# Performance work log

Hardware: AMD Instinct MI355X
Metric: run time of the kernel (lower is better)

## Reference

```python
import jax, jax.numpy as jnp
import numpy as np

N, D, H, B, TOPK, M, NLAB = 200000, 512, 512, 256, 2, 100, 2000

def setup_inputs():
    rng = np.random.default_rng(0)
    features = rng.standard_normal((N, D)).astype(np.float32) * 0.05
    labels = rng.integers(0, NLAB, size=N).astype(np.int32)
    # fixed-shape cluster membership table (replaces dynamic features[labels==lab]
    # + randperm subsampling to max_cluster_num=100 in the torch loop)
    order = np.argsort(labels, kind='stable').astype(np.int32)
    counts = np.bincount(labels, minlength=NLAB)
    offs = np.concatenate([[0], np.cumsum(counts)]).astype(np.int64)
    cluster_members = np.zeros((NLAB, M), np.int32)
    cluster_mask = np.zeros((NLAB, M), np.bool_)
    for c in range(NLAB):
        k = int(min(counts[c], M))
        cluster_members[c, :k] = order[offs[c]:offs[c] + k]
        cluster_mask[c, :k] = True
    indexes = rng.integers(0, N, size=B).astype(np.int32)
    # neighbors guaranteed != indexes so neighbor labels are never the -1 placeholder
    neighbors = ((indexes[:, None] + 1 + rng.integers(0, N - 1, size=(B, TOPK))) % N).astype(np.int32)
    all_pred = rng.random((B, TOPK)).astype(np.float32)
    # GraphConv weight [2D,H] (cat(self, agg)), classifier Linear-PReLU-Linear(2)
    W1 = (rng.standard_normal((2 * D, H)) / np.sqrt(2 * D)).astype(np.float32)
    b1 = np.zeros(H, np.float32)
    W2 = (rng.standard_normal((H, H)) / np.sqrt(H)).astype(np.float32)
    b2 = np.zeros(H, np.float32)
    prelu_a = np.full(H, 0.25, np.float32)  # PReLU default init
    W3 = (rng.standard_normal((H, 2)) / np.sqrt(H)).astype(np.float32)
    b3 = np.zeros(2, np.float32)
    arrs = dict(features=features, labels=labels, indexes=indexes, neighbors=neighbors,
                all_pred=all_pred, cluster_members=cluster_members, cluster_mask=cluster_mask,
                W1=W1, b1=b1, W2=W2, b2=b2, prelu_a=prelu_a, W3=W3, b3=b3)
    return {k: jnp.asarray(v) for k, v in arrs.items()}

def _gcnl_loss(features, labels, indexes, neighbors, all_pred, cluster_members, cluster_mask,
               W1, b1, W2, b2, prelu_a, W3, b3):
    Bn = indexes.shape[0]
    sel = all_pred >= all_pred[:, :1]                    # neighbor kept if pred[:topk] >= pred[0]
    cand = labels[neighbors]                             # [B,2] candidate labels
    dup = (cand[:, 1] == cand[:, 0]) & sel[:, 0]         # torch.unique over the <=2 selected labels
    valid = jnp.stack([sel[:, 0], sel[:, 1] & ~dup], axis=1)  # [B,2]
    members = cluster_members[cand]                      # [B,2,M]
    # labels[indexes[i]] = -1 in the loop => sample never in its own cluster
    mmask = cluster_mask[cand] & (members != indexes[:, None, None])
    mfeats = features[members] * mmask[..., None].astype(features.dtype)  # [B,2,M,D] zero-padded
    x0 = features[indexes]                               # [B,D]
    x0k = jnp.broadcast_to(x0[:, None, None, :], (Bn, TOPK, 1, x0.shape[-1]))
    x = jnp.concatenate([x0k, mfeats], axis=2)           # [B,2,M+1,D] = cat(self, cluster)
    # adj = x @ x.T ; only row 0 feeds the loss (pred[0]), zero-padded rows contribute 0
    a0 = jnp.einsum('bkd,bkmd->bkm', x[:, :, 0], x)      # [B,2,M+1] adjacency row 0
    agg0 = jnp.einsum('bkm,bkmd->bkd', a0, x)            # MeanAggregator (A @ x) row 0
    cat0 = jnp.concatenate([x[:, :, 0], agg0], axis=-1)  # [B,2,2D]
    h0 = jax.nn.relu(jnp.einsum('bkd,df->bkf', cat0, W1) + b1)  # GraphConv row 0
    z = jnp.einsum('bkf,fg->bkg', h0, W2) + b2
    z = jnp.where(z >= 0, z, prelu_a * z)                # PReLU
    logits = jnp.einsum('bkg,gc->bkc', z, W3) + b3       # [B,2,2]
    gt = (cand == -1).astype(jnp.int32)                  # labels[idx] was -1 during the loop
    logp = jax.nn.log_softmax(logits, axis=-1)
    ce = -jnp.take_along_axis(logp, gt[..., None], axis=-1)[..., 0]  # [B,2]
    loss = jnp.sum(ce * valid.astype(ce.dtype)) / Bn
    return loss * 10.0

def reference(features, labels, indexes, neighbors, all_pred, cluster_members, cluster_mask,
              W1, b1, W2, b2, prelu_a, W3, b3):
    return _gcnl_loss(features, labels, indexes, neighbors, all_pred, cluster_members, cluster_mask,
                      W1, b1, W2, b2, prelu_a, W3, b3)
```

## Files before the change

### kernel.cpp

```cpp
#include <hip/hip_runtime.h>
#include <math.h>

#define N_PTS 200000
#define D 512
#define H 512
#define BATCH 256
#define TOPK 2
#define MCAP 100
#define NLAB 2000

typedef __attribute__((ext_vector_type(8))) short bf16x8;
typedef __attribute__((ext_vector_type(4))) float f32x4;

__device__ inline unsigned short f2bf(float f) {
    unsigned int u = __float_as_uint(f);
    u += 0x7FFFu + ((u >> 16) & 1u);
    return (unsigned short)(u >> 16);
}

__global__ __launch_bounds__(512) void gather_prep_kernel(
    const float* __restrict__ features, const int* __restrict__ labels,
    const int* __restrict__ indexes, const int* __restrict__ neighbors,
    const float* __restrict__ all_pred, const int* __restrict__ cluster_members,
    const float* __restrict__ W1, const float* __restrict__ W2,
    unsigned short* __restrict__ W1t, unsigned short* __restrict__ W2t,
    unsigned short* __restrict__ cat0, float* __restrict__ validf, int* __restrict__ gts,
    float* __restrict__ out)
{
    int bid = blockIdx.x;
    int tid = threadIdx.x;

    if (bid >= 512) {
        __shared__ float tt[2][32][33];
        int t = (bid - 512) * 2 + (tid >> 8);
        int t256 = tid & 255;
        int tx = t256 & 31, ty = t256 >> 5;
        const float* src; unsigned short* dst; int R, C, bi;
        if (t < 512) { src = W1; dst = W1t; R = 1024; C = 512; bi = t; }
        else         { src = W2; dst = W2t; R = 512;  C = 512; bi = t - 512; }
        int nbc = C >> 5;
        int br = (bi / nbc) * 32, bc = (bi % nbc) * 32;
        int half = tid >> 8;
        #pragma unroll
        for (int i = 0; i < 32; i += 8)
            tt[half][ty + i][tx] = src[(size_t)(br + ty + i) * C + bc + tx];
        __syncthreads();
        #pragma unroll
        for (int i = 0; i < 32; i += 8)
            dst[(size_t)(bc + ty + i) * R + br + tx] = f2bf(tt[half][tx][ty + i]);
        return;
    }

    int bk = bid;
    int b = bk >> 1, k = bk & 1;
    int lane = tid & 63, w = tid >> 6;

    if (bk == 0 && tid == 0) out[0] = 0.0f;

    int idx  = indexes[b];
    int nb   = neighbors[b * TOPK + k];
    int c    = labels[nb];
    int lab0 = labels[0];

    const float4* frow0 = (const float4*)(features + (size_t)idx * D);
    float4 x0a = frow0[lane * 2];
    float4 x0b = frow0[lane * 2 + 1];

    float agg[8] = {0,0,0,0,0,0,0,0};

    for (int m = w; m < MCAP + 1; m += 8) {
        int row;
        if (m == 0) {
            row = idx;
        } else {
            int mm = m - 1;
            int r2 = cluster_members[c * MCAP + mm];
            if (r2 == 0 && !(c == lab0 && mm == 0)) continue;
            if (r2 == idx) continue;
            row = r2;
        }
        const float4* fr = (const float4*)(features + (size_t)row * D);
        float4 fa = fr[lane * 2];
        float4 fb = fr[lane * 2 + 1];
        float p = fa.x*x0a.x + fa.y*x0a.y + fa.z*x0a.z + fa.w*x0a.w
                + fb.x*x0b.x + fb.y*x0b.y + fb.z*x0b.z + fb.w*x0b.w;
        #pragma unroll
        for (int off = 32; off >= 1; off >>= 1) p += __shfl_xor(p, off);
        agg[0] += p * fa.x; agg[1] += p * fa.y; agg[2] += p * fa.z; agg[3] += p * fa.w;
        agg[4] += p * fb.x; agg[5] += p * fb.y; agg[6] += p * fb.z; agg[7] += p * fb.w;
    }

    __shared__ float aggl[8][D];
    #pragma unroll
    for (int j = 0; j < 8; ++j) aggl[w][lane * 8 + j] = agg[j];
    __syncthreads();

    unsigned short* crow = cat0 + (size_t)bk * (2 * D);
    if (w == 0) {
        union { unsigned short u[8]; uint4 q; } pk;
        pk.u[0] = f2bf(x0a.x); pk.u[1] = f2bf(x0a.y); pk.u[2] = f2bf(x0a.z); pk.u[3] = f2bf(x0a.w);
        pk.u[4] = f2bf(x0b.x); pk.u[5] = f2bf(x0b.y); pk.u[6] = f2bf(x0b.z); pk.u[7] = f2bf(x0b.w);
        ((uint4*)crow)[lane] = pk.q;
    }
    {
        int d = tid;
        float v = aggl[0][d] + aggl[1][d] + aggl[2][d] + aggl[3][d]
                + aggl[4][d] + aggl[5][d] + aggl[6][d] + aggl[7][d];
        crow[D + d] = f2bf(v);
    }
    if (tid == 0) {
        float p0 = all_pred[b * TOPK];
        float pk = all_pred[b * TOPK + k];
        int cand0 = labels[neighbors[b * TOPK]];
        bool valid;
        if (k == 0) valid = true;
        else        valid = (pk >= p0) && (c != cand0);
        validf[bk] = valid ? 1.0f : 0.0f;
        gts[bk] = (c == -1) ? 1 : 0;
    }
}

__global__ __launch_bounds__(512) void gemm_bf16(
    const unsigned short* __restrict__ A, const unsigned short* __restrict__ Bt,
    const float* __restrict__ bias, int N, int K, int act,
    const float* __restrict__ pa, float* __restrict__ Cf, unsigned short* __restrict__ Cb)
{
    int tid = threadIdx.x;
    int lane = tid & 63, w = tid >> 6;
    int nbn = N >> 5;
    int row0 = (blockIdx.x / nbn) * 32, col0 = (blockIdx.x % nbn) * 32;

    int r = lane & 15;
    int kg = (lane >> 4) * 8;
    int kb = w * (K >> 3);

    const unsigned short* Ar0 = A  + (size_t)(row0 + r) * K + kb + kg;
    const unsigned short* Ar1 = Ar0 + (size_t)16 * K;
    const unsigned short* Br0 = Bt + (size_t)(col0 + r) * K + kb + kg;
    const unsigned short* Br1 = Br0 + (size_t)16 * K;

    f32x4 acc00 = {0,0,0,0}, acc01 = {0,0,0,0}, acc10 = {0,0,0,0}, acc11 = {0,0,0,0};

    int kchunk = K >> 3;
    for (int ks = 0; ks < kchunk; ks += 32) {
        bf16x8 a0 = *(const bf16x8*)(Ar0 + ks);
        bf16x8 a1 = *(const bf16x8*)(Ar1 + ks);
        bf16x8 b0 = *(const bf16x8*)(Br0 + ks);
        bf16x8 b1 = *(const bf16x8*)(Br1 + ks);
        acc00 = __builtin_amdgcn_mfma_f32_16x16x32_bf16(a0, b0, acc00, 0, 0, 0);
        acc01 = __builtin_amdgcn_mfma_f32_16x16x32_bf16(a0, b1, acc01, 0, 0, 0);
        acc10 = __builtin_amdgcn_mfma_f32_16x16x32_bf16(a1, b0, acc10, 0, 0, 0);
        acc11 = __builtin_amdgcn_mfma_f32_16x16x32_bf16(a1, b1, acc11, 0, 0, 0);
    }

    __shared__ float red[8][32][33];
    int rbase = (lane >> 4) * 4, cbase = lane & 15;
    #pragma unroll
    for (int j = 0; j < 4; ++j) {
        red[w][rbase + j][cbase]           = acc00[j];
        red[w][rbase + j][16 + cbase]      = acc01[j];
        red[w][16 + rbase + j][cbase]      = acc10[j];
        red[w][16 + rbase + j][16 + cbase] = acc11[j];
    }
    __syncthreads();

    for (int e = tid; e < 1024; e += 512) {
        int rr = e >> 5, cc = e & 31;
        float v = red[0][rr][cc] + red[1][rr][cc] + red[2][rr][cc] + red[3][rr][cc]
                + red[4][rr][cc] + red[5][rr][cc] + red[6][rr][cc] + red[7][rr][cc];
        int gc = col0 + cc;
        v += bias[gc];
        if (act == 0) {
            v = fmaxf(v, 0.f);
            Cb[(size_t)(row0 + rr) * N + gc] = f2bf(v);
        } else {
            v = (v >= 0.f) ? v : pa[gc] * v;
            Cf[(size_t)(row0 + rr) * N + gc] = v;
        }
    }
}

__global__ __launch_bounds__(256) void final_kernel(
    const float* __restrict__ z, const float* __restrict__ W3, const float* __restrict__ b3,
    const float* __restrict__ validf, const int* __restrict__ gts, float* __restrict__ out)
{
    int w = threadIdx.x >> 6, lane = threadIdx.x & 63;
    int bk = blockIdx.x * 4 + w;
    const float* zr = z + (size_t)bk * H;
    const float4* z4 = (const float4*)zr;
    float4 za = z4[lane * 2], zb = z4[lane * 2 + 1];
    const float4* w4 = (const float4*)W3;
    float l0 = 0, l1 = 0;
    float4 wp;
    wp = w4[lane * 4 + 0]; l0 += za.x * wp.x + za.y * wp.z; l1 += za.x * wp.y + za.y * wp.w;
    wp = w4[lane * 4 + 1]; l0 += za.z * wp.x + za.w * wp.z; l1 += za.z * wp.y + za.w * wp.w;
    wp = w4[lane * 4 + 2]; l0 += zb.x * wp.x + zb.y * wp.z; l1 += zb.x * wp.y + zb.y * wp.w;
    wp = w4[lane * 4 + 3]; l0 += zb.z * wp.x + zb.w * wp.z; l1 += zb.z * wp.y + zb.w * wp.w;
    #pragma unroll
    for (int off = 32; off >= 1; off >>= 1) {
        l0 += __shfl_xor(l0, off);
        l1 += __shfl_xor(l1, off);
    }
    if (lane == 0) {
        l0 += b3[0]; l1 += b3[1];
        int gt = gts[bk];
        float mx = fmaxf(l0, l1);
        float lse = mx + logf(expf(l0 - mx) + expf(l1 - mx));
        float sel = (gt == 0) ? l0 : l1;
        float ce = lse - sel;
        atomicAdd(out, ce * validf[bk] * (10.0f / (float)BATCH));
    }
}

extern "C" void kernel_launch(void* const* d_in, const int* in_sizes, int n_in,
                              void* d_out, int out_size, void* d_ws, size_t ws_size,
                              hipStream_t stream) {
    const float* features        = (const float*)d_in[0];
    const int*   labels          = (const int*)d_in[1];
    const int*   indexes         = (const int*)d_in[2];
    const int*   neighbors       = (const int*)d_in[3];
    const float* all_pred        = (const float*)d_in[4];
    const int*   cluster_members = (const int*)d_in[5];
    const float* W1 = (const float*)d_in[7];
    const float* b1 = (const float*)d_in[8];
    const float* W2 = (const float*)d_in[9];
    const float* b2 = (const float*)d_in[10];
    const float* pa = (const float*)d_in[11];
    const float* W3 = (const float*)d_in[12];
    const float* b3 = (const float*)d_in[13];
    float* out = (float*)d_out;

    char* ws = (char*)d_ws;
    float*          validf = (float*)(ws + 8192);
    int*            gts    = (int*)(ws + 10240);
    unsigned short* W1t    = (unsigned short*)(ws + 12288);
    unsigned short* W2t    = (unsigned short*)(ws + 1060864);
    unsigned short* cat0b  = (unsigned short*)(ws + 1585152);
    unsigned short* h0b    = (unsigned short*)(ws + 2633728);
    float*          zbuf   = (float*)(ws + 3158016);

    gather_prep_kernel<<<896, 512, 0, stream>>>(
        features, labels, indexes, neighbors, all_pred, cluster_members,
        W1, W2, W1t, W2t, cat0b, validf, gts, out);
    gemm_bf16<<<256, 512, 0, stream>>>(cat0b, W1t, b1, 512, 1024, 0, pa, nullptr, h0b);
    gemm_bf16<<<256, 512, 0, stream>>>(h0b,   W2t, b2, 512, 512,  1, pa, zbuf, nullptr);
    final_kernel<<<128, 256, 0, stream>>>(zbuf, W3, b3, validf, gts, out);
}
```

Baseline: 42.08 us.

## Fuse classifier head and loss into second GEMM with last-block reduction

Removes the final kernel and the fp32 z buffer. The second GEMM epilogue now applies PReLU, multiplies by W3, and atomically accumulates per-row logits. A last-block-done counter then computes the cross-entropy and writes the loss directly. It also specializes the GEMMs with compile-time N and K and unrolls the k loop. The cost is many global atomics on logits plus a grid-wide fence and counter, which risk contention and make the float summation order nondeterministic.

```diff
diff --git a/kernel.cpp b/kernel.cpp
--- a/kernel.cpp
+++ b/kernel.cpp
@@ -7,7 +7,6 @@
 #define BATCH 256
 #define TOPK 2
 #define MCAP 100
-#define NLAB 2000
 
 typedef __attribute__((ext_vector_type(8))) short bf16x8;
 typedef __attribute__((ext_vector_type(4))) float f32x4;
@@ -25,7 +24,7 @@
     const float* __restrict__ W1, const float* __restrict__ W2,
     unsigned short* __restrict__ W1t, unsigned short* __restrict__ W2t,
     unsigned short* __restrict__ cat0, float* __restrict__ validf, int* __restrict__ gts,
-    float* __restrict__ out)
+    float* __restrict__ logits, int* __restrict__ done)
 {
     int bid = blockIdx.x;
     int tid = threadIdx.x;
@@ -55,7 +54,11 @@
     int b = bk >> 1, k = bk & 1;
     int lane = tid & 63, w = tid >> 6;
 
-    if (bk == 0 && tid == 0) out[0] = 0.0f;
+    if (bk == 0) {
+        logits[tid] = 0.0f;
+        logits[tid + 512] = 0.0f;
+        if (tid == 0) *done = 0;
+    }
 
     int idx  = indexes[b];
     int nb   = neighbors[b * TOPK + k];
@@ -103,10 +106,9 @@
         ((uint4*)crow)[lane] = pk.q;
     }
     {
-        int d = tid;
-        float v = aggl[0][d] + aggl[1][d] + aggl[2][d] + aggl[3][d]
-                + aggl[4][d] + aggl[5][d] + aggl[6][d] + aggl[7][d];
-        crow[D + d] = f2bf(v);
+        float v = aggl[0][tid] + aggl[1][tid] + aggl[2][tid] + aggl[3][tid]
+                + aggl[4][tid] + aggl[5][tid] + aggl[6][tid] + aggl[7][tid];
+        crow[D + tid] = f2bf(v);
     }
     if (tid == 0) {
         float p0 = all_pred[b * TOPK];
@@ -120,15 +122,14 @@
     }
 }
 
-__global__ __launch_bounds__(512) void gemm_bf16(
+__global__ __launch_bounds__(512) void gemm1_kernel(
     const unsigned short* __restrict__ A, const unsigned short* __restrict__ Bt,
-    const float* __restrict__ bias, int N, int K, int act,
-    const float* __restrict__ pa, float* __restrict__ Cf, unsigned short* __restrict__ Cb)
+    const float* __restrict__ bias, unsigned short* __restrict__ Cb)
 {
+    const int N = 512, K = 1024;
     int tid = threadIdx.x;
     int lane = tid & 63, w = tid >> 6;
-    int nbn = N >> 5;
-    int row0 = (blockIdx.x / nbn) * 32, col0 = (blockIdx.x % nbn) * 32;
+    int row0 = (blockIdx.x >> 4) * 32, col0 = (blockIdx.x & 15) * 32;
 
     int r = lane & 15;
     int kg = (lane >> 4) * 8;
@@ -141,8 +142,8 @@
 
     f32x4 acc00 = {0,0,0,0}, acc01 = {0,0,0,0}, acc10 = {0,0,0,0}, acc11 = {0,0,0,0};
 
-    int kchunk = K >> 3;
-    for (int ks = 0; ks < kchunk; ks += 32) {
+    #pragma unroll
+    for (int ks = 0; ks < (K >> 3); ks += 32) {
         bf16x8 a0 = *(const bf16x8*)(Ar0 + ks);
         bf16x8 a1 = *(const bf16x8*)(Ar1 + ks);
         bf16x8 b0 = *(const bf16x8*)(Br0 + ks);
@@ -164,51 +165,109 @@
     }
     __syncthreads();
 
+    #pragma unroll
     for (int e = tid; e < 1024; e += 512) {
         int rr = e >> 5, cc = e & 31;
         float v = red[0][rr][cc] + red[1][rr][cc] + red[2][rr][cc] + red[3][rr][cc]
                 + red[4][rr][cc] + red[5][rr][cc] + red[6][rr][cc] + red[7][rr][cc];
         int gc = col0 + cc;
-        v += bias[gc];
-        if (act == 0) {
-            v = fmaxf(v, 0.f);
-            Cb[(size_t)(row0 + rr) * N + gc] = f2bf(v);
-        } else {
-            v = (v >= 0.f) ? v : pa[gc] * v;
-            Cf[(size_t)(row0 + rr) * N + gc] = v;
+        v = fmaxf(v + bias[gc], 0.0f);
+        Cb[(size_t)(row0 + rr) * N + gc] = f2bf(v);
+    }
+}
+
+__global__ __launch_bounds__(512) void gemm2_kernel(
+    const unsigned short* __restrict__ A, const unsigned short* __restrict__ Bt,
+    const float* __restrict__ b2, const float* __restrict__ pa,
+    const float* __restrict__ W3, const float* __restrict__ b3,
+    const float* __restrict__ validf, const int* __restrict__ gts,
+    float* __restrict__ logits, int* __restrict__ done, float* __restrict__ out)
+{
+    const int K = 512;
+    int tid = threadIdx.x;
+    int lane = tid & 63, w = tid >> 6;
+    int row0 = (blockIdx.x >> 4) * 32, col0 = (blockIdx.x & 15) * 32;
+
+    int r = lane & 15;
+    int kg = (lane >> 4) * 8;
+    int kb = w * (K >> 3);
+
+    const unsigned short* Ar0 = A  + (size_t)(row0 + r) * K + kb + kg;
+    const unsigned short* Ar1 = Ar0 + (size_t)16 * K;
+    const unsigned short* Br0 = Bt + (size_t)(col0 + r) * K + kb + kg;
+    const unsigned short* Br1 = Br0 + (size_t)16 * K;
+
+    f32x4 acc00 = {0,0,0,0}, acc01 = {0,0,0,0}, acc10 = {0,0,0,0}, acc11 = {0,0,0,0};
+
+    #pragma unroll
+    for (int ks = 0; ks < (K >> 3); ks += 32) {
+        bf16x8 a0 = *(const bf16x8*)(Ar0 + ks);
+        bf16x8 a1 = *(const bf16x8*)(Ar1 + ks);
+        bf16x8 b0 = *(const bf16x8*)(Br0 + ks);
+        bf16x8 b1 = *(const bf16x8*)(Br1 + ks);
+        acc00 = __builtin_amdgcn_mfma_f32_16x16x32_bf16(a0, b0, acc00, 0, 0, 0);
+        acc01 = __builtin_amdgcn_mfma_f32_16x16x32_bf16(a0, b1, acc01, 0, 0, 0);
+        acc10 = __builtin_amdgcn_mfma_f32_16x16x32_bf16(a1, b0, acc10, 0, 0, 0);
+        acc11 = __builtin_amdgcn_mfma_f32_16x16x32_bf16(a1, b1, acc11, 0, 0, 0);
+    }
+
+    __shared__ float red[8][32][33];
+    int rbase = (lane >> 4) * 4, cbase = lane & 15;
+    #pragma unroll
+    for (int j = 0; j < 4; ++j) {
+        red[w][rbase + j][cbase]           = acc00[j];
+        red[w][rbase + j][16 + cbase]      = acc01[j];
+        red[w][16 + rbase + j][cbase]      = acc10[j];
+        red[w][16 + rbase + j][16 + cbase] = acc11[j];
+    }
+    __syncthreads();
+
+    #pragma unroll
+    for (int e = tid; e < 1024; e += 512) {
+        int rr = e >> 5, cc = e & 31;
+        float v = red[0][rr][cc] + red[1][rr][cc] + red[2][rr][cc] + red[3][rr][cc]
+                + red[4][rr][cc] + red[5][rr][cc] + red[6][rr][cc] + red[7][rr][cc];
+        int gc = col0 + cc;
+        v += b2[gc];
+        v = (v >= 0.0f) ? v : pa[gc] * v;
+        float p0 = v * W3[gc * 2];
+        float p1 = v * W3[gc * 2 + 1];
+        #pragma unroll
+        for (int off = 16; off >= 1; off >>= 1) {
+            p0 += __shfl_xor(p0, off);
+            p1 += __shfl_xor(p1, off);
         }
-    }
-}
-
-__global__ __launch_bounds__(256) void final_kernel(
-    const float* __restrict__ z, const float* __restrict__ W3, const float* __restrict__ b3,
-    const float* __restrict__ validf, const int* __restrict__ gts, float* __restrict__ out)
-{
-    int w = threadIdx.x >> 6, lane = threadIdx.x & 63;
-    int bk = blockIdx.x * 4 + w;
-    const float* zr = z + (size_t)bk * H;
-    const float4* z4 = (const float4*)zr;
-    float4 za = z4[lane * 2], zb = z4[lane * 2 + 1];
-    const float4* w4 = (const float4*)W3;
-    float l0 = 0, l1 = 0;
-    float4 wp;
-    wp = w4[lane * 4 + 0]; l0 += za.x * wp.x + za.y * wp.z; l1 += za.x * wp.y + za.y * wp.w;
-    wp = w4[lane * 4 + 1]; l0 += za.z * wp.x + za.w * wp.z; l1 += za.z * wp.y + za.w * wp.w;
-    wp = w4[lane * 4 + 2]; l0 += zb.x * wp.x + zb.y * wp.z; l1 += zb.x * wp.y + zb.y * wp.w;
-    wp = w4[lane * 4 + 3]; l0 += zb.z * wp.x + zb.w * wp.z; l1 += zb.z * wp.y + zb.w * wp.w;
-    #pragma unroll
-    for (int off = 32; off >= 1; off >>= 1) {
-        l0 += __shfl_xor(l0, off);
-        l1 += __shfl_xor(l1, off);
-    }
-    if (lane == 0) {
-        l0 += b3[0]; l1 += b3[1];
-        int gt = gts[bk];
+        if ((lane & 31) == 0) {
+            int brow = row0 + rr;
+            atomicAdd(&logits[brow * 2],     p0);
+            atomicAdd(&logits[brow * 2 + 1], p1);
+        }
+    }
+
+    __shared__ int islast;
+    __shared__ float fin[8];
+    __syncthreads();
+    __threadfence();
+    if (tid == 0) islast = (atomicAdd(done, 1) == 255) ? 1 : 0;
+    __syncthreads();
+    if (islast) {
+        int bk = tid;
+        float l0 = __hip_atomic_load(&logits[2 * bk],     __ATOMIC_RELAXED, __HIP_MEMORY_SCOPE_AGENT) + b3[0];
+        float l1 = __hip_atomic_load(&logits[2 * bk + 1], __ATOMIC_RELAXED, __HIP_MEMORY_SCOPE_AGENT) + b3[1];
         float mx = fmaxf(l0, l1);
         float lse = mx + logf(expf(l0 - mx) + expf(l1 - mx));
-        float sel = (gt == 0) ? l0 : l1;
-        float ce = lse - sel;
-        atomicAdd(out, ce * validf[bk] * (10.0f / (float)BATCH));
+        float sel = gts[bk] ? l1 : l0;
+        float ce = (lse - sel) * validf[bk];
+        #pragma unroll
+        for (int off = 32; off >= 1; off >>= 1) ce += __shfl_xor(ce, off);
+        if (lane == 0) fin[w] = ce;
+        __syncthreads();
+        if (tid == 0) {
+            float s = 0;
+            #pragma unroll
+            for (int q = 0; q < 8; ++q) s += fin[q];
+            out[0] = s * (10.0f / (float)BATCH);
+        }
     }
 }
 
@@ -231,18 +290,19 @@
     float* out = (float*)d_out;
 
     char* ws = (char*)d_ws;
+    float*          logits = (float*)ws;
+    int*            done   = (int*)(ws + 6144);
     float*          validf = (float*)(ws + 8192);
     int*            gts    = (int*)(ws + 10240);
     unsigned short* W1t    = (unsigned short*)(ws + 12288);
     unsigned short* W2t    = (unsigned short*)(ws + 1060864);
     unsigned short* cat0b  = (unsigned short*)(ws + 1585152);
     unsigned short* h0b    = (unsigned short*)(ws + 2633728);
-    float*          zbuf   = (float*)(ws + 3158016);
 
     gather_prep_kernel<<<896, 512, 0, stream>>>(
         features, labels, indexes, neighbors, all_pred, cluster_members,
-        W1, W2, W1t, W2t, cat0b, validf, gts, out);
-    gemm_bf16<<<256, 512, 0, stream>>>(cat0b, W1t, b1, 512, 1024, 0, pa, nullptr, h0b);
-    gemm_bf16<<<256, 512, 0, stream>>>(h0b,   W2t, b2, 512, 512,  1, pa, zbuf, nullptr);
-    final_kernel<<<128, 256, 0, stream>>>(zbuf, W3, b3, validf, gts, out);
-}
+        W1, W2, W1t, W2t, cat0b, validf, gts, logits, done);
+    gemm1_kernel<<<256, 512, 0, stream>>>(cat0b, W1t, b1, h0b);
+    gemm2_kernel<<<256, 512, 0, stream>>>(h0b, W2t, b2, pa, W3, b3,
+                                          validf, gts, logits, done, out);
+}
```

After: 64.82 us. 54.0% more time.
